# Kernel optimization log

Measured on AMD Instinct MI355X. Metric: run time of the kernel, lower is better.

The kernel has to match this reference:

```python
import jax, jax.numpy as jnp
import numpy as np

L, D, H, F_IN = 3, 256, 8, 5
HD = D // H
FF = 4 * D
EPS = 1e-5


def _layer_norm(x, g, b):
    mu = jnp.mean(x, axis=-1, keepdims=True)
    var = jnp.mean(jnp.square(x - mu), axis=-1, keepdims=True)
    return (x - mu) * jax.lax.rsqrt(var + EPS) * g + b


def setup_inputs() -> dict:
    key = jax.random.key(0)
    ks = jax.random.split(key, 20)
    s = 0.02
    inp = {
        'x': jax.random.normal(ks[0], (32, 512, F_IN), jnp.float32),
        'mask': jax.random.randint(ks[1], (32, 512), 0, 2) == 1,
        'Win': jax.random.normal(ks[2], (F_IN, D), jnp.float32) * s,
        'bin_': jnp.zeros((D,), jnp.float32),
        'Wq': jax.random.normal(ks[3], (L, D, D), jnp.float32) * s,
        'bq': jnp.zeros((L, D), jnp.float32),
        'Wk': jax.random.normal(ks[4], (L, D, D), jnp.float32) * s,
        'bk': jnp.zeros((L, D), jnp.float32),
        'Wv': jax.random.normal(ks[5], (L, D, D), jnp.float32) * s,
        'bv': jnp.zeros((L, D), jnp.float32),
        'Wo': jax.random.normal(ks[6], (L, D, D), jnp.float32) * s,
        'bo': jnp.zeros((L, D), jnp.float32),
        'g1': jnp.ones((L, D), jnp.float32),
        'b1': jnp.zeros((L, D), jnp.float32),
        'W1': jax.random.normal(ks[7], (L, D, FF), jnp.float32) * s,
        'c1': jnp.zeros((L, FF), jnp.float32),
        'W2': jax.random.normal(ks[8], (L, FF, D), jnp.float32) * s,
        'c2': jnp.zeros((L, D), jnp.float32),
        'g2': jnp.ones((L, D), jnp.float32),
        'b2': jnp.zeros((L, D), jnp.float32),
    }
    return inp


def reference(x, mask, Win, bin_, Wq, bq, Wk, bk, Wv, bv, Wo, bo, g1, b1, W1, c1, W2, c2, g2, b2):
    B, S, _ = x.shape
    scale = 1.0 / jnp.sqrt(jnp.float32(HD))
    h = x @ Win + bin_  # [B,S,D]
    kmask = mask[:, None, None, :]  # [B,1,1,S] key-padding mask
    for l in range(L):
        q = (h @ Wq[l] + bq[l]).reshape(B, S, H, HD).transpose(0, 2, 1, 3)
        k = (h @ Wk[l] + bk[l]).reshape(B, S, H, HD).transpose(0, 2, 1, 3)
        v = (h @ Wv[l] + bv[l]).reshape(B, S, H, HD).transpose(0, 2, 1, 3)
        scores = jnp.einsum('bhqd,bhkd->bhqk', q, k) * scale
        scores = jnp.where(kmask, -jnp.inf, scores)
        attn = jnp.nan_to_num(jax.nn.softmax(scores, axis=-1), nan=0.0)
        ao = jnp.einsum('bhqk,bhkd->bhqd', attn, v).transpose(0, 2, 1, 3).reshape(B, S, D)
        ao = ao @ Wo[l] + bo[l]
        h = _layer_norm(h + ao, g1[l], b1[l])
        ff = jax.nn.relu(h @ W1[l] + c1[l]) @ W2[l] + c2[l]
        h = _layer_norm(h + ff, g2[l], b2[l])
    return h
```

## Files before the change

### kernel.cpp

```cpp
#include <hip/hip_runtime.h>
#include <cstdint>

#define NLAYER 3
#define DMODEL 256
#define NHEAD 8
#define HEADD 32
#define FFDIM 1024
#define BATCH 32
#define SEQ 512
#define MTOK (BATCH*SEQ)

typedef __attribute__((ext_vector_type(8))) __bf16 bf16x8;
typedef __attribute__((ext_vector_type(4))) __bf16 bf16x4;
typedef __attribute__((ext_vector_type(4))) float f32x4;
typedef __attribute__((ext_vector_type(16))) float f32x16;

typedef __attribute__((address_space(1))) const uint8_t ga_t;
typedef __attribute__((address_space(3))) uint8_t la_t;
__device__ __forceinline__ void gll16(const void* g, void* l) {
    __builtin_amdgcn_global_load_lds((ga_t*)g, (la_t*)l, 16, 0, 0);
}

__global__ __launch_bounds__(256)
void prep_kernel(const float* __restrict__ Wq, const float* __restrict__ Wk,
                 const float* __restrict__ Wv, const float* __restrict__ Wo,
                 const float* __restrict__ W1, const float* __restrict__ W2,
                 const float* __restrict__ bq, const float* __restrict__ bk,
                 const float* __restrict__ bv,
                 __bf16* __restrict__ wqkv, __bf16* __restrict__ wot,
                 __bf16* __restrict__ w1t, __bf16* __restrict__ w2t,
                 float* __restrict__ bqkv)
{
    const int bid = blockIdx.x;
    const int tid = threadIdx.x;
    if (bid >= 3 * 768) {
        int idx = (bid - 3 * 768) * 256 + tid;
        int l = idx / 768, j = idx % 768;
        float v = (j < 256) ? bq[l * 256 + j]
                : (j < 512) ? bk[l * 256 + j - 256]
                            : bv[l * 256 + j - 512];
        bqkv[idx] = v;
        return;
    }
    const int l = bid / 768;
    const int rr = bid % 768;
    const float* src; __bf16* dst; int K, N, t;
    if (rr < 192) {
        int ty = rr >> 6; t = rr & 63;
        src = (ty == 0 ? Wq : ty == 1 ? Wk : Wv) + (size_t)l * 65536;
        dst = wqkv + (size_t)l * 768 * 256 + (size_t)ty * 65536;
        K = 256; N = 256;
    } else if (rr < 256) {
        t = rr - 192; src = Wo + (size_t)l * 65536; dst = wot + (size_t)l * 65536;
        K = 256; N = 256;
    } else if (rr < 512) {
        t = rr - 256; src = W1 + (size_t)l * 262144; dst = w1t + (size_t)l * 262144;
        K = 256; N = 1024;
    } else {
        t = rr - 512; src = W2 + (size_t)l * 262144; dst = w2t + (size_t)l * 262144;
        K = 1024; N = 256;
    }
    const int tn = N >> 5;
    const int tk = t / tn, tj = t % tn;
    __shared__ float tile[32][33];
    const int c = tid & 31, rbase = tid >> 5;
#pragma unroll
    for (int p = 0; p < 4; ++p) {
        int kr = rbase + p * 8;
        tile[kr][c] = src[(size_t)(tk * 32 + kr) * N + tj * 32 + c];
    }
    __syncthreads();
#pragma unroll
    for (int p = 0; p < 4; ++p) {
        int nr = rbase + p * 8;
        dst[(size_t)(tj * 32 + nr) * K + tk * 32 + c] = (__bf16)tile[c][nr];
    }
}

__global__ __launch_bounds__(256)
void inproj_kernel(const float* __restrict__ x, const float* __restrict__ Win,
                   const float* __restrict__ bin, float* __restrict__ h,
                   __bf16* __restrict__ h16)
{
    const int m = blockIdx.x;
    const int n = threadIdx.x;
    const float* xr = x + (size_t)m * 5;
    float acc = bin[n];
#pragma unroll
    for (int k = 0; k < 5; ++k) acc += xr[k] * Win[k * DMODEL + n];
    h[(size_t)m * DMODEL + n] = acc;
    h16[(size_t)m * DMODEL + n] = (__bf16)acc;
}

template<int RELU, int RES, int OBF>
__global__ __launch_bounds__(256, 3)
void gemm_kernel(const __bf16* __restrict__ A, const __bf16* __restrict__ Bt,
                 const float* __restrict__ bias, const float* __restrict__ res,
                 void* __restrict__ Cv, int M, int N, int K)
{
    __shared__ __bf16 As[128 * 64];
    __shared__ __bf16 Bs[128 * 64];
    const int tid = threadIdx.x;
    const int m0 = blockIdx.x * 128;
    const int n0 = blockIdx.y * 128;
    const int lane = tid & 63;
    const int wave = tid >> 6;
    const int wm = (wave & 1) * 64;
    const int wn = (wave >> 1) * 64;
    const int fr = lane & 15;
    const int quad = lane >> 4;
    const int lr = lane >> 3;
    const int qg = (lane & 7) ^ lr;

    const __bf16* Ab = A  + (size_t)(m0 + wave * 32 + lr) * K + qg * 8;
    const __bf16* Bb = Bt + (size_t)(n0 + wave * 32 + lr) * K + qg * 8;

    f32x4 acc[4][4];
#pragma unroll
    for (int i = 0; i < 4; ++i)
#pragma unroll
        for (int j = 0; j < 4; ++j)
#pragma unroll
            for (int r = 0; r < 4; ++r) acc[i][j][r] = 0.f;

    const int frs = fr & 7;

    for (int k0 = 0; k0 < K; k0 += 64) {
#pragma unroll
        for (int j = 0; j < 4; ++j) {
            gll16(Ab + (size_t)j * 8 * K + k0, As + (wave * 4 + j) * 512);
            gll16(Bb + (size_t)j * 8 * K + k0, Bs + (wave * 4 + j) * 512);
        }
        __syncthreads();
#pragma unroll
        for (int kk = 0; kk < 2; ++kk) {
            bf16x8 af[4], bfr[4];
#pragma unroll
            for (int i = 0; i < 4; ++i) {
                int row = wm + i * 16 + fr;
                af[i] = *(const bf16x8*)(As + row * 64 + (((kk * 4 + quad) ^ frs) * 8));
            }
#pragma unroll
            for (int j = 0; j < 4; ++j) {
                int row = wn + j * 16 + fr;
                bfr[j] = *(const bf16x8*)(Bs + row * 64 + (((kk * 4 + quad) ^ frs) * 8));
            }
#pragma unroll
            for (int i = 0; i < 4; ++i)
#pragma unroll
                for (int j = 0; j < 4; ++j)
                    acc[i][j] = __builtin_amdgcn_mfma_f32_16x16x32_bf16(
                        af[i], bfr[j], acc[i][j], 0, 0, 0);
        }
        __syncthreads();
    }

#pragma unroll
    for (int i = 0; i < 4; ++i) {
#pragma unroll
        for (int j = 0; j < 4; ++j) {
            const int gc = n0 + wn + j * 16 + fr;
            const float bv = bias[gc];
#pragma unroll
            for (int r = 0; r < 4; ++r) {
                const int gr = m0 + wm + i * 16 + quad * 4 + r;
                float v = acc[i][j][r] + bv;
                if (RES) v += res[(size_t)gr * N + gc];
                if (RELU) v = fmaxf(v, 0.f);
                if (OBF) ((__bf16*)Cv)[(size_t)gr * N + gc] = (__bf16)v;
                else     ((float*)Cv)[(size_t)gr * N + gc] = v;
            }
        }
    }
}

__global__ __launch_bounds__(1024)
void attn_kernel(const __bf16* __restrict__ qkv, const int* __restrict__ mask,
                 __bf16* __restrict__ ao)
{
    __shared__ __bf16 Ks[512 * 40];
    __shared__ __bf16 Vt[32 * 520];
    __shared__ __bf16 Pq[16 * 32 * 40];
    __shared__ float maskadd[512];

    const int b = blockIdx.x >> 3;
    const int h = blockIdx.x & 7;
    const int t = threadIdx.x;
    const int lane = t & 63;
    const int wave = t >> 6;
    const int cl = lane & 31;
    const int kh = lane >> 5;
    const float scale = 0.17677669529663687f;

    const size_t base = (size_t)b * SEQ * 768;

#pragma unroll
    for (int p = 0; p < 2; ++p) {
        int idx = p * 1024 + t;
        int key = idx >> 2, ch = idx & 3;
        bf16x8 kv = *(const bf16x8*)(qkv + base + (size_t)key * 768 + 256 + h * 32 + ch * 8);
        *(bf16x8*)(Ks + key * 40 + ch * 8) = kv;
        bf16x8 vv = *(const bf16x8*)(qkv + base + (size_t)key * 768 + 512 + h * 32 + ch * 8);
#pragma unroll
        for (int j = 0; j < 8; ++j) Vt[(ch * 8 + j) * 520 + key] = vv[j];
    }
    if (t < 512) maskadd[t] = mask[b * SEQ + t] ? -1e30f : 0.f;
    __syncthreads();

    const int q0 = wave * 32;
    const __bf16* qrow = qkv + base + (size_t)(q0 + cl) * 768 + h * 32;
    bf16x8 qf0 = *(const bf16x8*)(qrow + kh * 8);
    bf16x8 qf1 = *(const bf16x8*)(qrow + 16 + kh * 8);

    f32x16 oacc;
#pragma unroll
    for (int i = 0; i < 16; ++i) oacc[i] = 0.f;
    float lsum = 0.f;
    __bf16* Pw = Pq + wave * 32 * 40;

    for (int kt = 0; kt < SEQ; kt += 32) {
        bf16x8 kf0 = *(const bf16x8*)(Ks + (kt + cl) * 40 + kh * 8);
        bf16x8 kf1 = *(const bf16x8*)(Ks + (kt + cl) * 40 + 16 + kh * 8);
        f32x16 s;
#pragma unroll
        for (int i = 0; i < 16; ++i) s[i] = 0.f;
        s = __builtin_amdgcn_mfma_f32_32x32x16_bf16(kf0, qf0, s, 0, 0, 0);
        s = __builtin_amdgcn_mfma_f32_32x32x16_bf16(kf1, qf1, s, 0, 0, 0);
        float pv[16];
#pragma unroll
        for (int g = 0; g < 4; ++g) {
            f32x4 mv = *(const f32x4*)(maskadd + kt + 8 * g + 4 * kh);
#pragma unroll
            for (int r = 0; r < 4; ++r) {
                float e = __expf(s[g * 4 + r] * scale + mv[r]);
                pv[g * 4 + r] = e;
                lsum += e;
            }
        }
#pragma unroll
        for (int g = 0; g < 4; ++g) {
            bf16x4 pb;
#pragma unroll
            for (int r = 0; r < 4; ++r) pb[r] = (__bf16)pv[g * 4 + r];
            *(bf16x4*)(Pw + cl * 40 + 8 * g + 4 * kh) = pb;
        }
        bf16x8 pf0 = *(const bf16x8*)(Pw + cl * 40 + kh * 8);
        bf16x8 pf1 = *(const bf16x8*)(Pw + cl * 40 + 16 + kh * 8);
        bf16x8 vf0 = *(const bf16x8*)(Vt + cl * 520 + kt + kh * 8);
        bf16x8 vf1 = *(const bf16x8*)(Vt + cl * 520 + kt + 16 + kh * 8);
        oacc = __builtin_amdgcn_mfma_f32_32x32x16_bf16(vf0, pf0, oacc, 0, 0, 0);
        oacc = __builtin_amdgcn_mfma_f32_32x32x16_bf16(vf1, pf1, oacc, 0, 0, 0);
    }

    lsum += __shfl_xor(lsum, 32);
    const float inv = (lsum > 0.f) ? 1.f / lsum : 0.f;
    __bf16* orow = ao + (size_t)(b * SEQ + q0 + cl) * DMODEL + h * 32;
#pragma unroll
    for (int g = 0; g < 4; ++g) {
        bf16x4 w;
#pragma unroll
        for (int r = 0; r < 4; ++r) w[r] = (__bf16)(oacc[g * 4 + r] * inv);
        *(bf16x4*)(orow + 8 * g + 4 * kh) = w;
    }
}

__global__ __launch_bounds__(256)
void ln_kernel(const float* __restrict__ rin, const float* __restrict__ g,
               const float* __restrict__ be, float* __restrict__ out,
               __bf16* __restrict__ out16)
{
    const int row = blockIdx.x * 4 + (threadIdx.x >> 6);
    const int lane = threadIdx.x & 63;
    const float* x = rin + (size_t)row * DMODEL + lane * 4;
    f32x4 v = *(const f32x4*)x;
    float s = v[0] + v[1] + v[2] + v[3];
    float ss = v[0] * v[0] + v[1] * v[1] + v[2] * v[2] + v[3] * v[3];
#pragma unroll
    for (int off = 1; off < 64; off <<= 1) {
        s  += __shfl_xor(s, off, 64);
        ss += __shfl_xor(ss, off, 64);
    }
    const float mu = s * (1.f / DMODEL);
    const float var = ss * (1.f / DMODEL) - mu * mu;
    const float rs = rsqrtf(var + 1e-5f);
    f32x4 gv = *(const f32x4*)(g + lane * 4);
    f32x4 bv = *(const f32x4*)(be + lane * 4);
    f32x4 y;
#pragma unroll
    for (int i = 0; i < 4; ++i) y[i] = (v[i] - mu) * rs * gv[i] + bv[i];
    *(f32x4*)(out + (size_t)row * DMODEL + lane * 4) = y;
    if (out16) {
        bf16x4 yb;
#pragma unroll
        for (int i = 0; i < 4; ++i) yb[i] = (__bf16)y[i];
        *(bf16x4*)(out16 + (size_t)row * DMODEL + lane * 4) = yb;
    }
}

extern "C" void kernel_launch(void* const* d_in, const int* in_sizes, int n_in,
                              void* d_out, int out_size, void* d_ws, size_t ws_size,
                              hipStream_t stream)
{
    const float* x   = (const float*)d_in[0];
    const int*   mask= (const int*)d_in[1];
    const float* Win = (const float*)d_in[2];
    const float* bin = (const float*)d_in[3];
    const float* Wq  = (const float*)d_in[4];
    const float* bq  = (const float*)d_in[5];
    const float* Wk  = (const float*)d_in[6];
    const float* bk  = (const float*)d_in[7];
    const float* Wv  = (const float*)d_in[8];
    const float* bv  = (const float*)d_in[9];
    const float* Wo  = (const float*)d_in[10];
    const float* bo  = (const float*)d_in[11];
    const float* g1  = (const float*)d_in[12];
    const float* b1  = (const float*)d_in[13];
    const float* W1  = (const float*)d_in[14];
    const float* c1  = (const float*)d_in[15];
    const float* W2  = (const float*)d_in[16];
    const float* c2  = (const float*)d_in[17];
    const float* g2  = (const float*)d_in[18];
    const float* b2  = (const float*)d_in[19];

    char* ws = (char*)d_ws;
    size_t off = 0;
    auto alloc = [&](size_t bytes) -> void* {
        void* p = ws + off;
        off += (bytes + 255) & ~(size_t)255;
        return p;
    };
    float*  h    = (float*)alloc((size_t)MTOK * 256 * 4);
    __bf16* h16  = (__bf16*)alloc((size_t)MTOK * 256 * 2);
    float*  rbuf = (float*)alloc((size_t)MTOK * 256 * 4);
    __bf16* u    = (__bf16*)alloc((size_t)MTOK * 1024 * 2);
    __bf16* qkv  = u;
    __bf16* ffT  = u;
    __bf16* ao   = (__bf16*)alloc((size_t)MTOK * 256 * 2);
    __bf16* wqkv = (__bf16*)alloc((size_t)3 * 768 * 256 * 2);
    __bf16* wot  = (__bf16*)alloc((size_t)3 * 256 * 256 * 2);
    __bf16* w1t  = (__bf16*)alloc((size_t)3 * 1024 * 256 * 2);
    __bf16* w2t  = (__bf16*)alloc((size_t)3 * 256 * 1024 * 2);
    float*  bqkv = (float*)alloc((size_t)3 * 768 * 4);

    prep_kernel<<<dim3(2313), dim3(256), 0, stream>>>(
        Wq, Wk, Wv, Wo, W1, W2, bq, bk, bv, wqkv, wot, w1t, w2t, bqkv);
    inproj_kernel<<<dim3(MTOK), dim3(256), 0, stream>>>(x, Win, bin, h, h16);

    for (int l = 0; l < NLAYER; ++l) {
        gemm_kernel<0, 0, 1><<<dim3(128, 6), dim3(256), 0, stream>>>(
            h16, wqkv + (size_t)l * 768 * 256, bqkv + l * 768, nullptr,
            qkv, MTOK, 768, 256);
        attn_kernel<<<dim3(256), dim3(1024), 0, stream>>>(qkv, mask, ao);
        gemm_kernel<0, 1, 0><<<dim3(128, 2), dim3(256), 0, stream>>>(
            ao, wot + (size_t)l * 65536, bo + l * 256, h, rbuf, MTOK, 256, 256);
        ln_kernel<<<dim3(MTOK / 4), dim3(256), 0, stream>>>(
            rbuf, g1 + l * 256, b1 + l * 256, h, h16);
        gemm_kernel<1, 0, 1><<<dim3(128, 8), dim3(256), 0, stream>>>(
            h16, w1t + (size_t)l * 262144, c1 + l * 1024, nullptr,
            ffT, MTOK, 1024, 256);
        gemm_kernel<0, 1, 0><<<dim3(128, 2), dim3(256), 0, stream>>>(
            ffT, w2t + (size_t)l * 262144, c2 + l * 256, h, rbuf, MTOK, 256, 1024);
        ln_kernel<<<dim3(MTOK / 4), dim3(256), 0, stream>>>(
            rbuf, g2 + l * 256, b2 + l * 256,
            (l == 2) ? (float*)d_out : h, (l == 2) ? nullptr : h16);
    }
}
```

Before: 397.1 us.

## Fuse residual add and LayerNorm into full-row output-projection GEMMs, keep hidden in bf16

Adds a GEMM kernel whose block covers 64 rows and all 256 output columns, so the bias, residual add and LayerNorm can be done in its epilogue with a cross-wave reduction through shared memory. This removes the separate LN kernels and the fp32 intermediate buffers. The residual stream is now kept only in bf16, ping-ponging between two buffers, which cuts memory traffic. The cost is lower precision on the residual path, and a K=1024 FF2 GEMM that now runs only 256 blocks with a larger B tile, which may lower occupancy.

```diff
diff --git a/kernel.cpp b/kernel.cpp
--- a/kernel.cpp
+++ b/kernel.cpp
@@ -79,8 +79,7 @@
 
 __global__ __launch_bounds__(256)
 void inproj_kernel(const float* __restrict__ x, const float* __restrict__ Win,
-                   const float* __restrict__ bin, float* __restrict__ h,
-                   __bf16* __restrict__ h16)
+                   const float* __restrict__ bin, __bf16* __restrict__ h16)
 {
     const int m = blockIdx.x;
     const int n = threadIdx.x;
@@ -88,15 +87,14 @@
     float acc = bin[n];
 #pragma unroll
     for (int k = 0; k < 5; ++k) acc += xr[k] * Win[k * DMODEL + n];
-    h[(size_t)m * DMODEL + n] = acc;
     h16[(size_t)m * DMODEL + n] = (__bf16)acc;
 }
 
-template<int RELU, int RES, int OBF>
+template<int RELU>
 __global__ __launch_bounds__(256, 3)
 void gemm_kernel(const __bf16* __restrict__ A, const __bf16* __restrict__ Bt,
-                 const float* __restrict__ bias, const float* __restrict__ res,
-                 void* __restrict__ Cv, int M, int N, int K)
+                 const float* __restrict__ bias,
+                 __bf16* __restrict__ C, int M, int N, int K)
 {
     __shared__ __bf16 As[128 * 64];
     __shared__ __bf16 Bs[128 * 64];
@@ -165,10 +163,126 @@
             for (int r = 0; r < 4; ++r) {
                 const int gr = m0 + wm + i * 16 + quad * 4 + r;
                 float v = acc[i][j][r] + bv;
-                if (RES) v += res[(size_t)gr * N + gc];
                 if (RELU) v = fmaxf(v, 0.f);
-                if (OBF) ((__bf16*)Cv)[(size_t)gr * N + gc] = (__bf16)v;
-                else     ((float*)Cv)[(size_t)gr * N + gc] = v;
+                C[(size_t)gr * N + gc] = (__bf16)v;
+            }
+        }
+    }
+}
+
+template<int LAST>
+__global__ __launch_bounds__(256, 2)
+void gemm_ln_kernel(const __bf16* __restrict__ A, const __bf16* __restrict__ Bt,
+                    const float* __restrict__ bias, const __bf16* __restrict__ res,
+                    const float* __restrict__ g, const float* __restrict__ be,
+                    __bf16* __restrict__ out16, float* __restrict__ out32, int K)
+{
+    __shared__ __bf16 As[64 * 64];
+    __shared__ __bf16 Bs[256 * 64];
+    __shared__ float red[64 * 8];
+    const int tid = threadIdx.x;
+    const int m0 = blockIdx.x * 64;
+    const int lane = tid & 63;
+    const int wave = tid >> 6;
+    const int wn = wave * 64;
+    const int fr = lane & 15;
+    const int quad = lane >> 4;
+    const int lr = lane >> 3;
+    const int qg = (lane & 7) ^ lr;
+    const int frs = fr & 7;
+
+    const __bf16* Ab = A  + (size_t)(m0 + wave * 16 + lr) * K + qg * 8;
+    const __bf16* Bb = Bt + (size_t)(wave * 64 + lr) * K + qg * 8;
+
+    f32x4 acc[4][4];
+#pragma unroll
+    for (int i = 0; i < 4; ++i)
+#pragma unroll
+        for (int j = 0; j < 4; ++j)
+#pragma unroll
+            for (int r = 0; r < 4; ++r) acc[i][j][r] = 0.f;
+
+    for (int k0 = 0; k0 < K; k0 += 64) {
+#pragma unroll
+        for (int p = 0; p < 2; ++p)
+            gll16(Ab + (size_t)p * 8 * K + k0, As + (wave * 2 + p) * 512);
+#pragma unroll
+        for (int p = 0; p < 8; ++p)
+            gll16(Bb + (size_t)p * 8 * K + k0, Bs + (wave * 8 + p) * 512);
+        __syncthreads();
+#pragma unroll
+        for (int kk = 0; kk < 2; ++kk) {
+            bf16x8 af[4], bfr[4];
+#pragma unroll
+            for (int i = 0; i < 4; ++i) {
+                int row = i * 16 + fr;
+                af[i] = *(const bf16x8*)(As + row * 64 + (((kk * 4 + quad) ^ frs) * 8));
+            }
+#pragma unroll
+            for (int j = 0; j < 4; ++j) {
+                int row = wn + j * 16 + fr;
+                bfr[j] = *(const bf16x8*)(Bs + row * 64 + (((kk * 4 + quad) ^ frs) * 8));
+            }
+#pragma unroll
+            for (int i = 0; i < 4; ++i)
+#pragma unroll
+                for (int j = 0; j < 4; ++j)
+                    acc[i][j] = __builtin_amdgcn_mfma_f32_16x16x32_bf16(
+                        af[i], bfr[j], acc[i][j], 0, 0, 0);
+        }
+        __syncthreads();
+    }
+
+    float bv[4];
+#pragma unroll
+    for (int j = 0; j < 4; ++j) bv[j] = bias[wn + j * 16 + fr];
+
+#pragma unroll
+    for (int i = 0; i < 4; ++i) {
+#pragma unroll
+        for (int r = 0; r < 4; ++r) {
+            const int row = i * 16 + quad * 4 + r;
+            float ps = 0.f, pq = 0.f;
+#pragma unroll
+            for (int j = 0; j < 4; ++j) {
+                const int gc = wn + j * 16 + fr;
+                float v = acc[i][j][r] + bv[j]
+                        + (float)res[(size_t)(m0 + row) * DMODEL + gc];
+                acc[i][j][r] = v;
+                ps += v;
+                pq += v * v;
+            }
+#pragma unroll
+            for (int off = 1; off < 16; off <<= 1) {
+                ps += __shfl_xor(ps, off, 64);
+                pq += __shfl_xor(pq, off, 64);
+            }
+            if (fr == 0) {
+                red[row * 8 + wave * 2]     = ps;
+                red[row * 8 + wave * 2 + 1] = pq;
+            }
+        }
+    }
+    __syncthreads();
+
+#pragma unroll
+    for (int i = 0; i < 4; ++i) {
+#pragma unroll
+        for (int r = 0; r < 4; ++r) {
+            const int row = i * 16 + quad * 4 + r;
+            f32x4 a = *(const f32x4*)(red + row * 8);
+            f32x4 b2 = *(const f32x4*)(red + row * 8 + 4);
+            const float s  = a[0] + a[2] + b2[0] + b2[2];
+            const float sq = a[1] + a[3] + b2[1] + b2[3];
+            const float mu = s * (1.f / DMODEL);
+            const float var = sq * (1.f / DMODEL) - mu * mu;
+            const float rs = rsqrtf(var + 1e-5f);
+#pragma unroll
+            for (int j = 0; j < 4; ++j) {
+                const int gc = wn + j * 16 + fr;
+                float y = (acc[i][j][r] - mu) * rs * g[gc] + be[gc];
+                if (LAST) out32[(size_t)(m0 + row) * DMODEL + gc] = y;
+                else      out16[(size_t)(m0 + row) * DMODEL + gc] = (__bf16)y;
             }
         }
     }
@@ -261,39 +375,6 @@
 #pragma unroll
         for (int r = 0; r < 4; ++r) w[r] = (__bf16)(oacc[g * 4 + r] * inv);
         *(bf16x4*)(orow + 8 * g + 4 * kh) = w;
-    }
-}
-
-__global__ __launch_bounds__(256)
-void ln_kernel(const float* __restrict__ rin, const float* __restrict__ g,
-               const float* __restrict__ be, float* __restrict__ out,
-               __bf16* __restrict__ out16)
-{
-    const int row = blockIdx.x * 4 + (threadIdx.x >> 6);
-    const int lane = threadIdx.x & 63;
-    const float* x = rin + (size_t)row * DMODEL + lane * 4;
-    f32x4 v = *(const f32x4*)x;
-    float s = v[0] + v[1] + v[2] + v[3];
-    float ss = v[0] * v[0] + v[1] * v[1] + v[2] * v[2] + v[3] * v[3];
-#pragma unroll
-    for (int off = 1; off < 64; off <<= 1) {
-        s  += __shfl_xor(s, off, 64);
-        ss += __shfl_xor(ss, off, 64);
-    }
-    const float mu = s * (1.f / DMODEL);
-    const float var = ss * (1.f / DMODEL) - mu * mu;
-    const float rs = rsqrtf(var + 1e-5f);
-    f32x4 gv = *(const f32x4*)(g + lane * 4);
-    f32x4 bv = *(const f32x4*)(be + lane * 4);
-    f32x4 y;
-#pragma unroll
-    for (int i = 0; i < 4; ++i) y[i] = (v[i] - mu) * rs * gv[i] + bv[i];
-    *(f32x4*)(out + (size_t)row * DMODEL + lane * 4) = y;
-    if (out16) {
-        bf16x4 yb;
-#pragma unroll
-        for (int i = 0; i < 4; ++i) yb[i] = (__bf16)y[i];
-        *(bf16x4*)(out16 + (size_t)row * DMODEL + lane * 4) = yb;
     }
 }
 
@@ -329,9 +410,8 @@
         off += (bytes + 255) & ~(size_t)255;
         return p;
     };
-    float*  h    = (float*)alloc((size_t)MTOK * 256 * 4);
-    __bf16* h16  = (__bf16*)alloc((size_t)MTOK * 256 * 2);
-    float*  rbuf = (float*)alloc((size_t)MTOK * 256 * 4);
+    __bf16* hA   = (__bf16*)alloc((size_t)MTOK * 256 * 2);
+    __bf16* hB   = (__bf16*)alloc((size_t)MTOK * 256 * 2);
     __bf16* u    = (__bf16*)alloc((size_t)MTOK * 1024 * 2);
     __bf16* qkv  = u;
     __bf16* ffT  = u;
@@ -344,24 +424,25 @@
 
     prep_kernel<<<dim3(2313), dim3(256), 0, stream>>>(
         Wq, Wk, Wv, Wo, W1, W2, bq, bk, bv, wqkv, wot, w1t, w2t, bqkv);
-    inproj_kernel<<<dim3(MTOK), dim3(256), 0, stream>>>(x, Win, bin, h, h16);
+    inproj_kernel<<<dim3(MTOK), dim3(256), 0, stream>>>(x, Win, bin, hA);
 
     for (int l = 0; l < NLAYER; ++l) {
-        gemm_kernel<0, 0, 1><<<dim3(128, 6), dim3(256), 0, stream>>>(
-            h16, wqkv + (size_t)l * 768 * 256, bqkv + l * 768, nullptr,
-            qkv, MTOK, 768, 256);
+        gemm_kernel<0><<<dim3(128, 6), dim3(256), 0, stream>>>(
+            hA, wqkv + (size_t)l * 768 * 256, bqkv + l * 768, qkv, MTOK, 768, 256);
         attn_kernel<<<dim3(256), dim3(1024), 0, stream>>>(qkv, mask, ao);
-        gemm_kernel<0, 1, 0><<<dim3(128, 2), dim3(256), 0, stream>>>(
-            ao, wot + (size_t)l * 65536, bo + l * 256, h, rbuf, MTOK, 256, 256);
-        ln_kernel<<<dim3(MTOK / 4), dim3(256), 0, stream>>>(
-            rbuf, g1 + l * 256, b1 + l * 256, h, h16);
-        gemm_kernel<1, 0, 1><<<dim3(128, 8), dim3(256), 0, stream>>>(
-            h16, w1t + (size_t)l * 262144, c1 + l * 1024, nullptr,
-            ffT, MTOK, 1024, 256);
-        gemm_kernel<0, 1, 0><<<dim3(128, 2), dim3(256), 0, stream>>>(
-            ffT, w2t + (size_t)l * 262144, c2 + l * 256, h, rbuf, MTOK, 256, 1024);
-        ln_kernel<<<dim3(MTOK / 4), dim3(256), 0, stream>>>(
-            rbuf, g2 + l * 256, b2 + l * 256,
-            (l == 2) ? (float*)d_out : h, (l == 2) ? nullptr : h16);
-    }
-}
+        gemm_ln_kernel<0><<<dim3(MTOK / 64), dim3(256), 0, stream>>>(
+            ao, wot + (size_t)l * 65536, bo + l * 256, hA,
+            g1 + l * 256, b1 + l * 256, hB, nullptr, 256);
+        gemm_kernel<1><<<dim3(128, 8), dim3(256), 0, stream>>>(
+            hB, w1t + (size_t)l * 262144, c1 + l * 1024, ffT, MTOK, 1024, 256);
+        if (l == 2) {
+            gemm_ln_kernel<1><<<dim3(MTOK / 64), dim3(256), 0, stream>>>(
+                ffT, w2t + (size_t)l * 262144, c2 + l * 256, hB,
+                g2 + l * 256, b2 + l * 256, nullptr, (float*)d_out, 1024);
+        } else {
+            gemm_ln_kernel<0><<<dim3(MTOK / 64), dim3(256), 0, stream>>>(
+                ffT, w2t + (size_t)l * 262144, c2 + l * 256, hB,
+                g2 + l * 256, b2 + l * 256, hA, nullptr, 1024);
+        }
+    }
+}
```

After: 392.0 us. No clear change (-1.3%).
